# Kernel tuning notes

Measured on AMD Instinct MI355X. Metric: run time of the kernel, lower is better.

The kernel has to match this reference:

```python
import jax, jax.numpy as jnp
import numpy as np

H = 256; HEADS = 4; DH = H // HEADS; LAYERS = 2; FEAT = 7
N = 20000; L = 32; E = 640000


def _ln(x, g, b, eps=1e-5):
    mu = x.mean(-1, keepdims=True)
    var = ((x - mu) ** 2).mean(-1, keepdims=True)
    return (x - mu) / jnp.sqrt(var + eps) * g + b


def setup_inputs() -> dict:
    key = jax.random.key(0)
    ks = jax.random.split(key, 12)
    s = 0.05
    nrm = lambda k, shp: jax.random.normal(k, shp, jnp.float32) * s
    return {
        "literal_reprs": jax.random.normal(ks[0], (N, L, H), jnp.float32),
        "clause_features": jax.random.uniform(ks[1], (N, FEAT), jnp.float32),
        "mask": jax.random.randint(ks[2], (N, L), 0, 2) == 1,
        "adjacency": jax.random.randint(ks[3], (2, E), 0, N),
        "pe_w1": nrm(ks[4], (FEAT, H)), "pe_b1": jnp.zeros((H,), jnp.float32),
        "pe_w2": nrm(ks[5], (H, H)), "pe_b2": jnp.zeros((H,), jnp.float32),
        "attn_in_w": nrm(ks[6], (H, 3 * H)), "attn_in_b": jnp.zeros((3 * H,), jnp.float32),
        "attn_out_w": nrm(ks[7], (H, H)), "attn_out_b": jnp.zeros((H,), jnp.float32),
        "attn_ln_g": jnp.ones((H,), jnp.float32), "attn_ln_b": jnp.zeros((H,), jnp.float32),
        "gate_w": nrm(ks[8], (2 * H, H)), "gate_b": jnp.zeros((H,), jnp.float32),
        "trans_w": nrm(ks[9], (2 * H, H)), "trans_b": jnp.zeros((H,), jnp.float32),
        "fus_ln_g": jnp.ones((H,), jnp.float32), "fus_ln_b": jnp.zeros((H,), jnp.float32),
        "mp_w": nrm(ks[10], (LAYERS, 2 * H, H)), "mp_b": jnp.zeros((LAYERS, H), jnp.float32),
        "mp_ln_g": jnp.ones((LAYERS, H), jnp.float32), "mp_ln_b": jnp.zeros((LAYERS, H), jnp.float32),
    }


def reference(literal_reprs, clause_features, mask, adjacency,
              pe_w1, pe_b1, pe_w2, pe_b2,
              attn_in_w, attn_in_b, attn_out_w, attn_out_b,
              attn_ln_g, attn_ln_b, gate_w, gate_b, trans_w, trans_b,
              fus_ln_g, fus_ln_b, mp_w, mp_b, mp_ln_g, mp_ln_b):
    n, l, h = literal_reprs.shape
    # clause property encoder (shared by query and fusion path)
    enc = jnp.maximum(clause_features @ pe_w1 + pe_b1, 0.0) @ pe_w2 + pe_b2  # (N, H)
    # single-query multi-head attention over literals
    wq, wk, wv = attn_in_w[:, :H], attn_in_w[:, H:2 * H], attn_in_w[:, 2 * H:]
    bq, bk, bv = attn_in_b[:H], attn_in_b[H:2 * H], attn_in_b[2 * H:]
    q = ((enc @ wq + bq) * (1.0 / np.sqrt(DH))).reshape(n, HEADS, DH)
    k = (literal_reprs @ wk + bk).reshape(n, l, HEADS, DH)
    v = (literal_reprs @ wv + bv).reshape(n, l, HEADS, DH)
    scores = jnp.einsum('nhd,nlhd->nhl', q, k)
    kpm = ~mask  # True = masked out
    all_masked = jnp.all(kpm, axis=1)
    kpm = kpm.at[:, 0].set(jnp.where(all_masked, False, kpm[:, 0]))  # unmask pos 0 for fully-masked rows
    scores = jnp.where(kpm[:, None, :], -jnp.inf, scores)
    attn = jax.nn.softmax(scores, axis=-1)
    ctx = jnp.einsum('nhl,nlhd->nhd', attn, v).reshape(n, h) @ attn_out_w + attn_out_b
    ctx = jnp.where(all_masked[:, None], 0.0, ctx)  # zero fully-masked rows
    attn_repr = _ln(ctx + enc, attn_ln_g, attn_ln_b)
    # masked mean-pool residual
    mf = mask.astype(literal_reprs.dtype)[:, :, None]
    lit_mean = (literal_reprs * mf).sum(1) / jnp.maximum(mf.sum(1), 1.0)
    attn_repr = attn_repr + lit_mean
    # gated fusion
    combined = jnp.concatenate([attn_repr, enc], axis=-1)
    gate = jax.nn.sigmoid(combined @ gate_w + gate_b)
    transform = combined @ trans_w + trans_b
    x = _ln(gate * attn_repr + (1.0 - gate) * transform, fus_ln_g, fus_ln_b)
    # inter-clause message passing
    src, dst = adjacency[0], adjacency[1]
    ones = jnp.ones((src.shape[0],), x.dtype)
    for i in range(LAYERS):
        agg = jax.ops.segment_sum(x[src], dst, num_segments=n)
        cnt = jax.ops.segment_sum(ones, dst, num_segments=n)
        agg = agg / jnp.maximum(cnt, 1.0)[:, None]
        upd = jnp.maximum(jnp.concatenate([x, agg], axis=-1) @ mp_w[i] + mp_b[i], 0.0)
        x = _ln(x + upd, mp_ln_g[i], mp_ln_b[i])
    return x
```

## Files before the change

### kernel.cpp

```cpp
#include <hip/hip_runtime.h>
#include <math.h>

#define H 256
#define L 32
#define HEADS 4
#define FEAT 7
#define LN_EPS 1e-5f

typedef __attribute__((ext_vector_type(8))) short bf16x8;
typedef __attribute__((ext_vector_type(4))) float f32x4;
typedef __attribute__((ext_vector_type(4))) float fvec4;

__device__ __forceinline__ float wave_reduce_sum64(float v) {
#pragma unroll
  for (int m = 32; m >= 1; m >>= 1) v += __shfl_xor(v, m, 64);
  return v;
}

__device__ __forceinline__ short bf16rne(float f) {
  unsigned u = __float_as_uint(f);
  unsigned r = (u + 0x7FFFu + ((u >> 16) & 1u)) >> 16;
  return (short)r;
}

__device__ __forceinline__ float bf2f(short s) {
  return __uint_as_float(((unsigned)(unsigned short)s) << 16);
}

__global__ __launch_bounds__(256) void k_prep(
    const float* __restrict__ pe_w2, const float* __restrict__ aiw, const float* __restrict__ aow,
    const float* __restrict__ aib, const float* __restrict__ aob,
    const float* __restrict__ gate_w, const float* __restrict__ trans_w, const float* __restrict__ mp_w,
    short* __restrict__ w2P, short* __restrict__ wqpP, short* __restrict__ wbigP,
    short* __restrict__ gwP, short* __restrict__ twP, short* __restrict__ mp0P, short* __restrict__ mp1P,
    float* __restrict__ bias_p, float* __restrict__ bias_out, int* __restrict__ hist, int n) {
  const int bb = blockIdx.x;
  const int tid = threadIdx.x;
  if (bb < 32) {
    const int t = bb * 256 + tid;
    const int lane = t & 63;
    const int ks = (t >> 6) & 7;
    const int tcol = (t >> 6) >> 3;
    const int j = tcol * 16 + (lane & 15);
    const int k0 = ks * 32 + (lane >> 4) * 8;
    short v[8];
#pragma unroll
    for (int i = 0; i < 8; ++i) v[i] = bf16rne(pe_w2[(size_t)(k0 + i) * 256 + j]);
    *(int4*)&w2P[(size_t)t * 8] = *(int4*)v;
  } else if (bb < 160) {
    const int t = (bb - 32) * 256 + tid;
    const int lane = t & 63;
    const int ks = (t >> 6) & 7;
    const int tcol = t >> 9;
    const int col = tcol * 16 + (lane & 15);
    const int h = col >> 8, c = col & 255;
    const int k0 = ks * 32 + (lane >> 4) * 8;
    short v[8];
#pragma unroll
    for (int i = 0; i < 8; ++i) {
      const int k = k0 + i;
      float s = 0.f;
      for (int d = 0; d < 64; d += 4) {
        const float4 qa = *(const float4*)&aiw[(size_t)k * 768 + h * 64 + d];
        const float4 ka = *(const float4*)&aiw[(size_t)c * 768 + 256 + h * 64 + d];
        s = fmaf(qa.x, ka.x, fmaf(qa.y, ka.y, fmaf(qa.z, ka.z, fmaf(qa.w, ka.w, s))));
      }
      v[i] = bf16rne(0.125f * s);
    }
    *(int4*)&wqpP[(size_t)t * 8] = *(int4*)v;
  } else if (bb < 288) {
    const int t = (bb - 160) * 256 + tid;
    const int lane = t & 63;
    const int ks = (t >> 6) & 31;
    const int tcol = t >> 11;
    const int j = tcol * 16 + (lane & 15);
    const int k0 = ks * 32 + (lane >> 4) * 8;
    short v[8];
#pragma unroll
    for (int i = 0; i < 8; ++i) {
      const int k = k0 + i;
      const int c = k >> 2, h = k & 3;
      float s = 0.f;
      for (int d = 0; d < 64; ++d)
        s = fmaf(aiw[(size_t)c * 768 + 512 + h * 64 + d], aow[(size_t)(h * 64 + d) * 256 + j], s);
      v[i] = bf16rne(s);
    }
    *(int4*)&wbigP[(size_t)t * 8] = *(int4*)v;
  } else if (bb < 544) {
    const int sub = bb - 288;
    const int mi = sub >> 6;
    const float* W = (mi == 0) ? gate_w : (mi == 1) ? trans_w : (mi == 2) ? mp_w : (mp_w + 512 * 256);
    short* P = (mi == 0) ? gwP : (mi == 1) ? twP : (mi == 2) ? mp0P : mp1P;
    const int t = (sub & 63) * 256 + tid;
    const int lane = t & 63;
    const int ks = (t >> 6) & 15;
    const int tcol = (t >> 6) >> 4;
    const int j = tcol * 16 + (lane & 15);
    const int k0 = ks * 32 + (lane >> 4) * 8;
    short v[8];
#pragma unroll
    for (int i = 0; i < 8; ++i) v[i] = bf16rne(W[(size_t)(k0 + i) * 256 + j]);
    *(int4*)&P[(size_t)t * 8] = *(int4*)v;
  } else if (bb < 548) {
    const int col = (bb - 544) * 256 + tid;
    const int h = col >> 8, c = col & 255;
    float s = 0.f;
    for (int d = 0; d < 64; ++d)
      s = fmaf(aib[h * 64 + d], aiw[(size_t)c * 768 + 256 + h * 64 + d], s);
    bias_p[col] = 0.125f * s;
  } else if (bb == 548) {
    const int j = tid;
    float s = aob[j];
    for (int e2 = 0; e2 < 256; ++e2) s = fmaf(aib[512 + e2], aow[(size_t)e2 * 256 + j], s);
    bias_out[j] = s;
  } else {
    const int i = (bb - 549) * 256 + tid;
    if (i < n) hist[i] = 0;
  }
}

__global__ __launch_bounds__(256) void k_enc_mfma(
    const float* __restrict__ cf, const float* __restrict__ pe_w1, const float* __restrict__ pe_b1,
    const short* __restrict__ w2P, const float* __restrict__ pe_b2,
    const short* __restrict__ wqpP, const float* __restrict__ bias_p,
    short* __restrict__ enc_bf16, short* __restrict__ p_bf16, int n) {
  __shared__ float cfs[32][FEAT];
  __shared__ short h1[32][264];
  __shared__ short encS[32][264];
  const int tid = threadIdx.x;
  const int lane = tid & 63, w = tid >> 6;
  const int n0 = blockIdx.x * 32;
  for (int idx = tid; idx < 32 * FEAT; idx += 256) cfs[idx / FEAT][idx % FEAT] = cf[(size_t)n0 * FEAT + idx];
  __syncthreads();
  {
    const int j = tid;
    float wv[FEAT];
#pragma unroll
    for (int f = 0; f < FEAT; ++f) wv[f] = pe_w1[f * H + j];
    const float b1v = pe_b1[j];
    for (int r = 0; r < 32; ++r) {
      float s = b1v;
#pragma unroll
      for (int f = 0; f < FEAT; ++f) s = fmaf(cfs[r][f], wv[f], s);
      h1[r][j] = bf16rne(fmaxf(s, 0.f));
    }
  }
  __syncthreads();
  const int arow = lane & 15;
  const int koff = (lane >> 4) * 8;
  {
    f32x4 acc[2][4];
#pragma unroll
    for (int rt = 0; rt < 2; ++rt)
#pragma unroll
      for (int ct = 0; ct < 4; ++ct) acc[rt][ct] = (f32x4)0.f;
#pragma unroll
    for (int ks = 0; ks < 8; ++ks) {
      const int k0 = ks * 32 + koff;
      const bf16x8 a0 = *(const bf16x8*)&h1[arow][k0];
      const bf16x8 a1 = *(const bf16x8*)&h1[16 + arow][k0];
#pragma unroll
      for (int ct = 0; ct < 4; ++ct) {
        const size_t fo = (((size_t)(w * 4 + ct) * 8 + ks) * 64 + lane) * 8;
        const bf16x8 b = *(const bf16x8*)&w2P[fo];
        acc[0][ct] = __builtin_amdgcn_mfma_f32_16x16x32_bf16(a0, b, acc[0][ct], 0, 0, 0);
        acc[1][ct] = __builtin_amdgcn_mfma_f32_16x16x32_bf16(a1, b, acc[1][ct], 0, 0, 0);
      }
    }
#pragma unroll
    for (int rt = 0; rt < 2; ++rt)
#pragma unroll
      for (int ct = 0; ct < 4; ++ct) {
        const int col = w * 64 + ct * 16 + (lane & 15);
        const float b2v = pe_b2[col];
#pragma unroll
        for (int i = 0; i < 4; ++i) {
          const int row = rt * 16 + (lane >> 4) * 4 + i;
          const short bv = bf16rne(acc[rt][ct][i] + b2v);
          encS[row][col] = bv;
          enc_bf16[(size_t)(n0 + row) * H + col] = bv;
        }
      }
  }
  __syncthreads();
#pragma unroll
  for (int chunk = 0; chunk < 2; ++chunk) {
    f32x4 acc[2][8];
#pragma unroll
    for (int rt = 0; rt < 2; ++rt)
#pragma unroll
      for (int c8 = 0; c8 < 8; ++c8) acc[rt][c8] = (f32x4)0.f;
#pragma unroll
    for (int ks = 0; ks < 8; ++ks) {
      const int k0 = ks * 32 + koff;
      const bf16x8 a0 = *(const bf16x8*)&encS[arow][k0];
      const bf16x8 a1 = *(const bf16x8*)&encS[16 + arow][k0];
#pragma unroll
      for (int c8 = 0; c8 < 8; ++c8) {
        const int tcol = w * 16 + chunk * 8 + c8;
        const size_t fo = (((size_t)tcol * 8 + ks) * 64 + lane) * 8;
        const bf16x8 b = *(const bf16x8*)&wqpP[fo];
        acc[0][c8] = __builtin_amdgcn_mfma_f32_16x16x32_bf16(a0, b, acc[0][c8], 0, 0, 0);
        acc[1][c8] = __builtin_amdgcn_mfma_f32_16x16x32_bf16(a1, b, acc[1][c8], 0, 0, 0);
      }
    }
#pragma unroll
    for (int rt = 0; rt < 2; ++rt)
#pragma unroll
      for (int c8 = 0; c8 < 8; ++c8) {
        const int col = w * 256 + (chunk * 8 + c8) * 16 + (lane & 15);
        const float bp = bias_p[col];
#pragma unroll
        for (int i = 0; i < 4; ++i) {
          const int row = rt * 16 + (lane >> 4) * 4 + i;
          p_bf16[(size_t)(n0 + row) * 1024 + col] = bf16rne(acc[rt][c8][i] + bp);
        }
      }
  }
}

__global__ __launch_bounds__(256) void k_attn(
    const float* __restrict__ lit, const int* __restrict__ mask,
    const short* __restrict__ p_in, short* __restrict__ m_out,
    short* __restrict__ litmean_bf, int* __restrict__ flags, int n) {
  __shared__ short lit_bs[32][264];
  __shared__ float attn_s[32][4];
  __shared__ int validS[32];
  __shared__ int nvalidS;
  const int j = threadIdx.x;
  const int nn = blockIdx.x;
  const fvec4* litrow4 = (const fvec4*)(lit + (size_t)nn * (L * H));
#pragma unroll
  for (int t = 0; t < 8; ++t) {
    const int q = t * 256 + j;
    const int idx = q << 2;
    const int r = idx >> 8, c = idx & 255;
    const fvec4 f = __builtin_nontemporal_load(&litrow4[q]);
    short4 hv;
    hv.x = bf16rne(f.x); hv.y = bf16rne(f.y); hv.z = bf16rne(f.z); hv.w = bf16rne(f.w);
    *(short4*)&lit_bs[r][c] = hv;
  }
  if (j < 32) validS[j] = (mask[(size_t)nn * L + j] != 0) ? 1 : 0;
  __syncthreads();
  if (j == 0) {
    int c = 0;
#pragma unroll
    for (int l = 0; l < 32; ++l) c += validS[l];
    nvalidS = c;
  }
  __syncthreads();
  const int nvalid = nvalidS;
  const bool allm = (nvalid == 0);
  if (j < 64) {
    const int lane = j;
    f32x4 sc0 = (f32x4)0.f, sc1 = (f32x4)0.f;
    const int hh = lane & 3;
    const int krow = (lane >> 4) * 8;
    const short* prow = p_in + (size_t)nn * 1024 + hh * 256;
#pragma unroll
    for (int ks = 0; ks < 8; ++ks) {
      const bf16x8 a = *(const bf16x8*)&prow[ks * 32 + krow];
      const bf16x8 b0 = *(const bf16x8*)&lit_bs[lane & 15][ks * 32 + krow];
      const bf16x8 b1 = *(const bf16x8*)&lit_bs[16 + (lane & 15)][ks * 32 + krow];
      sc0 = __builtin_amdgcn_mfma_f32_16x16x32_bf16(a, b0, sc0, 0, 0, 0);
      sc1 = __builtin_amdgcn_mfma_f32_16x16x32_bf16(a, b1, sc1, 0, 0, 0);
    }
    if (lane < 16) {
      const int l0 = lane, l1 = 16 + lane;
      const bool ok0 = validS[l0] || (allm && l0 == 0);
      const bool ok1 = validS[l1] != 0;
#pragma unroll
      for (int i = 0; i < 4; ++i) {
        float s0 = ok0 ? sc0[i] : -INFINITY;
        float s1 = ok1 ? sc1[i] : -INFINITY;
        float mx = fmaxf(s0, s1);
#pragma unroll
        for (int m = 8; m >= 1; m >>= 1) mx = fmaxf(mx, __shfl_xor(mx, m, 16));
        float e0 = ok0 ? __expf(s0 - mx) : 0.f;
        float e1 = ok1 ? __expf(s1 - mx) : 0.f;
        float sm = e0 + e1;
#pragma unroll
        for (int m = 8; m >= 1; m >>= 1) sm += __shfl_xor(sm, m, 16);
        const float inv = 1.f / sm;
        attn_s[l0][i] = e0 * inv;
        attn_s[l1][i] = e1 * inv;
      }
    }
  }
  __syncthreads();
  {
    const float inv = 1.f / fmaxf((float)nvalid, 1.f);
    float lm = 0.f;
    float mm0 = 0.f, mm1 = 0.f, mm2 = 0.f, mm3 = 0.f;
#pragma unroll
    for (int l = 0; l < 32; ++l) {
      const float lv = bf2f(lit_bs[l][j]);
      if (validS[l]) lm += lv;
      const float4 av = *(const float4*)&attn_s[l][0];
      mm0 = fmaf(av.x, lv, mm0);
      mm1 = fmaf(av.y, lv, mm1);
      mm2 = fmaf(av.z, lv, mm2);
      mm3 = fmaf(av.w, lv, mm3);
    }
    litmean_bf[(size_t)nn * H + j] = bf16rne(lm * inv);
    short4 mv;
    mv.x = bf16rne(mm0); mv.y = bf16rne(mm1); mv.z = bf16rne(mm2); mv.w = bf16rne(mm3);
    *(short4*)&m_out[(size_t)nn * 1024 + j * 4] = mv;
  }
  if (j == 0) flags[nn] = allm ? 1 : 0;
}

__global__ __launch_bounds__(256) void k_fused(
    const short* __restrict__ m_bf16, const short* __restrict__ wbigP, const float* __restrict__ bias_out,
    const short* __restrict__ enc_bf16, const short* __restrict__ litmean_bf, const int* __restrict__ flags,
    const float* __restrict__ ag, const float* __restrict__ ab,
    const short* __restrict__ gwP, const short* __restrict__ twP,
    const float* __restrict__ gb, const float* __restrict__ tb,
    const float* __restrict__ fg, const float* __restrict__ fb,
    short* __restrict__ xout_bf, int n) {
  __shared__ short As[32][520];
  __shared__ float v_s[32][260];
  __shared__ float mu_s[32], sg_s[32];
  __shared__ int flagS[32];
  const int tid = threadIdx.x;
  const int lane = tid & 63, w = tid >> 6;
  const int n0 = blockIdx.x * 32;
  for (int q8 = tid; q8 < 32 * 32; q8 += 256) {
    const int idx = q8 << 3;
    const int r = idx >> 8, c = idx & 255;
    *(int4*)&As[r][256 + c] = *(const int4*)&enc_bf16[(size_t)(n0 + r) * H + c];
  }
  if (tid < 32) flagS[tid] = flags[n0 + tid];
  const int arow = lane & 15;
  const int koff = (lane >> 4) * 8;
  f32x4 acc[2][4];
#pragma unroll
  for (int rt = 0; rt < 2; ++rt)
#pragma unroll
    for (int ct = 0; ct < 4; ++ct) acc[rt][ct] = (f32x4)0.f;
#pragma unroll 8
  for (int ks = 0; ks < 32; ++ks) {
    const size_t abase = (size_t)(n0 + arow) * 1024 + ks * 32 + koff;
    const bf16x8 a0 = *(const bf16x8*)&m_bf16[abase];
    const bf16x8 a1 = *(const bf16x8*)&m_bf16[abase + 16 * 1024];
#pragma unroll
    for (int ct = 0; ct < 4; ++ct) {
      const size_t fo = (((size_t)(w * 4 + ct) * 32 + ks) * 64 + lane) * 8;
      const bf16x8 bw = *(const bf16x8*)&wbigP[fo];
      acc[0][ct] = __builtin_amdgcn_mfma_f32_16x16x32_bf16(a0, bw, acc[0][ct], 0, 0, 0);
      acc[1][ct] = __builtin_amdgcn_mfma_f32_16x16x32_bf16(a1, bw, acc[1][ct], 0, 0, 0);
    }
  }
  __syncthreads();
#pragma unroll
  for (int rt = 0; rt < 2; ++rt)
#pragma unroll
    for (int ct = 0; ct < 4; ++ct) {
      const int col = w * 64 + ct * 16 + (lane & 15);
      const float bo = bias_out[col];
#pragma unroll
      for (int i = 0; i < 4; ++i) {
        const int row = rt * 16 + (lane >> 4) * 4 + i;
        const float o = flagS[row] ? 0.f : (acc[rt][ct][i] + bo);
        v_s[row][col] = o + bf2f(As[row][256 + col]);
      }
    }
  __syncthreads();
  for (int r = w; r < 32; r += 4) {
    float ps = 0.f, pq = 0.f;
#pragma unroll
    for (int t = 0; t < 4; ++t) {
      float v = v_s[r][lane + 64 * t];
      ps += v;
      pq = fmaf(v, v, pq);
    }
    ps = wave_reduce_sum64(ps);
    pq = wave_reduce_sum64(pq);
    if (lane == 0) {
      float mu = ps * (1.f / H);
      mu_s[r] = mu;
      sg_s[r] = rsqrtf(pq * (1.f / H) - mu * mu + LN_EPS);
    }
  }
  __syncthreads();
  {
    const float agv = ag[tid], abv = ab[tid];
    for (int r = 0; r < 32; ++r) {
      const float val = (v_s[r][tid] - mu_s[r]) * sg_s[r] * agv + abv +
                        bf2f(litmean_bf[(size_t)(n0 + r) * H + tid]);
      As[r][tid] = bf16rne(val);
    }
  }
  __syncthreads();
  f32x4 accg[2][4], acct[2][4];
#pragma unroll
  for (int rt = 0; rt < 2; ++rt)
#pragma unroll
    for (int ct = 0; ct < 4; ++ct) { accg[rt][ct] = (f32x4)0.f; acct[rt][ct] = (f32x4)0.f; }
#pragma unroll 4
  for (int ks = 0; ks < 16; ++ks) {
    const int k0 = ks * 32 + koff;
    const bf16x8 a0 = *(const bf16x8*)&As[arow][k0];
    const bf16x8 a1 = *(const bf16x8*)&As[16 + arow][k0];
#pragma unroll
    for (int ct = 0; ct < 4; ++ct) {
      const size_t fo = (((size_t)(w * 4 + ct) * 16 + ks) * 64 + lane) * 8;
      const bf16x8 bg = *(const bf16x8*)&gwP[fo];
      const bf16x8 bt = *(const bf16x8*)&twP[fo];
      accg[0][ct] = __builtin_amdgcn_mfma_f32_16x16x32_bf16(a0, bg, accg[0][ct], 0, 0, 0);
      accg[1][ct] = __builtin_amdgcn_mfma_f32_16x16x32_bf16(a1, bg, accg[1][ct], 0, 0, 0);
      acct[0][ct] = __builtin_amdgcn_mfma_f32_16x16x32_bf16(a0, bt, acct[0][ct], 0, 0, 0);
      acct[1][ct] = __builtin_amdgcn_mfma_f32_16x16x32_bf16(a1, bt, acct[1][ct], 0, 0, 0);
    }
  }
#pragma unroll
  for (int rt = 0; rt < 2; ++rt)
#pragma unroll
    for (int ct = 0; ct < 4; ++ct) {
      const int col = w * 64 + ct * 16 + (lane & 15);
      const float gbv = gb[col], tbv = tb[col];
#pragma unroll
      for (int i = 0; i < 4; ++i) {
        const int rl = rt * 16 + (lane >> 4) * 4 + i;
        const float gate = 1.f / (1.f + __expf(-(accg[rt][ct][i] + gbv)));
        const float tr = acct[rt][ct][i] + tbv;
        const float a = bf2f(As[rl][col]);
        v_s[rl][col] = fmaf(gate, a - tr, tr);
      }
    }
  __syncthreads();
  for (int r = w; r < 32; r += 4) {
    float ps = 0.f, pq = 0.f;
#pragma unroll
    for (int t = 0; t < 4; ++t) {
      float v = v_s[r][lane + 64 * t];
      ps += v;
      pq = fmaf(v, v, pq);
    }
    ps = wave_reduce_sum64(ps);
    pq = wave_reduce_sum64(pq);
    if (lane == 0) {
      float mu = ps * (1.f / H);
      mu_s[r] = mu;
      sg_s[r] = rsqrtf(pq * (1.f / H) - mu * mu + LN_EPS);
    }
  }
  __syncthreads();
  {
    const float fgv = fg[tid], fbv = fb[tid];
    for (int r = 0; r < 32; ++r)
      xout_bf[(size_t)(n0 + r) * H + tid] = bf16rne((v_s[r][tid] - mu_s[r]) * sg_s[r] * fgv + fbv);
  }
}

__global__ __launch_bounds__(256) void k_mp_mfma(
    const short* __restrict__ xin_bf, const short* __restrict__ agg_bf,
    const short* __restrict__ wP, const float* __restrict__ bias,
    const float* __restrict__ g, const float* __restrict__ b,
    float* __restrict__ xout_f32, short* __restrict__ xout_bf, int n) {
  __shared__ float v_s[32][260];
  __shared__ float mu_s[32], sg_s[32];
  const int tid = threadIdx.x;
  const int lane = tid & 63, w = tid >> 6;
  const int n0 = blockIdx.x * 32;
  const int arow = lane & 15;
  const int koff = (lane >> 4) * 8;
  f32x4 acc[2][4];
#pragma unroll
  for (int rt = 0; rt < 2; ++rt)
#pragma unroll
    for (int ct = 0; ct < 4; ++ct) acc[rt][ct] = (f32x4)0.f;
  const short* xr0 = xin_bf + (size_t)(n0 + arow) * H;
  const short* xr1 = xin_bf + (size_t)(n0 + 16 + arow) * H;
  const short* gr0 = agg_bf + (size_t)(n0 + arow) * H;
  const short* gr1 = agg_bf + (size_t)(n0 + 16 + arow) * H;
#pragma unroll
  for (int ks = 0; ks < 8; ++ks) {
    const bf16x8 a0 = *(const bf16x8*)&xr0[ks * 32 + koff];
    const bf16x8 a1 = *(const bf16x8*)&xr1[ks * 32 + koff];
#pragma unroll
    for (int ct = 0; ct < 4; ++ct) {
      const size_t fo = (((size_t)(w * 4 + ct) * 16 + ks) * 64 + lane) * 8;
      const bf16x8 bw = *(const bf16x8*)&wP[fo];
      acc[0][ct] = __builtin_amdgcn_mfma_f32_16x16x32_bf16(a0, bw, acc[0][ct], 0, 0, 0);
      acc[1][ct] = __builtin_amdgcn_mfma_f32_16x16x32_bf16(a1, bw, acc[1][ct], 0, 0, 0);
    }
  }
#pragma unroll
  for (int ks = 8; ks < 16; ++ks) {
    const bf16x8 a0 = *(const bf16x8*)&gr0[(ks - 8) * 32 + koff];
    const bf16x8 a1 = *(const bf16x8*)&gr1[(ks - 8) * 32 + koff];
#pragma unroll
    for (int ct = 0; ct < 4; ++ct) {
      const size_t fo = (((size_t)(w * 4 + ct) * 16 + ks) * 64 + lane) * 8;
      const bf16x8 bw = *(const bf16x8*)&wP[fo];
      acc[0][ct] = __builtin_amdgcn_mfma_f32_16x16x32_bf16(a0, bw, acc[0][ct], 0, 0, 0);
      acc[1][ct] = __builtin_amdgcn_mfma_f32_16x16x32_bf16(a1, bw, acc[1][ct], 0, 0, 0);
    }
  }
#pragma unroll
  for (int rt = 0; rt < 2; ++rt)
#pragma unroll
    for (int ct = 0; ct < 4; ++ct) {
      const int col = w * 64 + ct * 16 + (lane & 15);
      const float bsv = bias[col];
#pragma unroll
      for (int i = 0; i < 4; ++i) {
        const int rl = rt * 16 + (lane >> 4) * 4 + i;
        const float u = fmaxf(acc[rt][ct][i] + bsv, 0.f);
        v_s[rl][col] = bf2f(xin_bf[(size_t)(n0 + rl) * H + col]) + u;
      }
    }
  __syncthreads();
  for (int r = w; r < 32; r += 4) {
    float ps = 0.f, pq = 0.f;
#pragma unroll
    for (int t = 0; t < 4; ++t) {
      float v = v_s[r][lane + 64 * t];
      ps += v;
      pq = fmaf(v, v, pq);
    }
    ps = wave_reduce_sum64(ps);
    pq = wave_reduce_sum64(pq);
    if (lane == 0) {
      float mu = ps * (1.f / H);
      mu_s[r] = mu;
      sg_s[r] = rsqrtf(pq * (1.f / H) - mu * mu + LN_EPS);
    }
  }
  __syncthreads();
  const float gv = g[tid], bv = b[tid];
  for (int r = 0; r < 32; ++r) {
    const float val = (v_s[r][tid] - mu_s[r]) * sg_s[r] * gv + bv;
    if (xout_f32) xout_f32[(size_t)(n0 + r) * H + tid] = val;
    if (xout_bf) xout_bf[(size_t)(n0 + r) * H + tid] = bf16rne(val);
  }
}

__global__ void k_hist(const int* __restrict__ dst, int* __restrict__ hist, int e) {
  int i = blockIdx.x * blockDim.x + threadIdx.x;
  if (i < e) atomicAdd(&hist[dst[i]], 1);
}

__global__ __launch_bounds__(1024) void k_scan(
    const int* __restrict__ hist, int* __restrict__ row_ptr, int* __restrict__ cursor, int n, int e) {
  __shared__ int part[1024];
  const int t = threadIdx.x;
  const int chunk = (n + 1023) / 1024;
  const int lo = t * chunk;
  const int hi = min(lo + chunk, n);
  int s = 0;
  for (int i = lo; i < hi; ++i) s += hist[i];
  part[t] = s;
  __syncthreads();
  for (int d = 1; d < 1024; d <<= 1) {
    int v = (t >= d) ? part[t - d] : 0;
    __syncthreads();
    part[t] += v;
    __syncthreads();
  }
  int run = (t > 0) ? part[t - 1] : 0;
  for (int i = lo; i < hi; ++i) {
    row_ptr[i] = run;
    cursor[i] = run;
    run += hist[i];
  }
  if (t == 1023) row_ptr[n] = e;
}

__global__ void k_fill(const int* __restrict__ adj, int* __restrict__ cursor,
                       int* __restrict__ edge_src, int e) {
  int i = blockIdx.x * blockDim.x + threadIdx.x;
  if (i < e) {
    int s = adj[i], d = adj[e + i];
    int pos = atomicAdd(&cursor[d], 1);
    edge_src[pos] = s;
  }
}

__global__ __launch_bounds__(256) void k_gather(
    const short* __restrict__ x, const int* __restrict__ edge_src, const int* __restrict__ row_ptr,
    short* __restrict__ agg, int n) {
  const int wid = threadIdx.x >> 6;
  const int lane = threadIdx.x & 63;
  const int d = blockIdx.x * 4 + wid;
  if (d >= n) return;
  const int beg = row_ptr[d], end = row_ptr[d + 1];
  float4 acc = {0.f, 0.f, 0.f, 0.f};
  int i = beg;
  for (; i + 8 <= end; i += 8) {
    short4 v[8];
#pragma unroll
    for (int u = 0; u < 8; ++u) {
      const int s = edge_src[i + u];
      v[u] = *(const short4*)(x + (size_t)s * H + lane * 4);
    }
#pragma unroll
    for (int u = 0; u < 8; ++u) {
      acc.x += bf2f(v[u].x);
      acc.y += bf2f(v[u].y);
      acc.z += bf2f(v[u].z);
      acc.w += bf2f(v[u].w);
    }
  }
  for (; i < end; ++i) {
    const int s = edge_src[i];
    const short4 v = *(const short4*)(x + (size_t)s * H + lane * 4);
    acc.x += bf2f(v.x); acc.y += bf2f(v.y); acc.z += bf2f(v.z); acc.w += bf2f(v.w);
  }
  const float inv = 1.f / fmaxf((float)(end - beg), 1.f);
  short4 o;
  o.x = bf16rne(acc.x * inv); o.y = bf16rne(acc.y * inv);
  o.z = bf16rne(acc.z * inv); o.w = bf16rne(acc.w * inv);
  *(short4*)(agg + (size_t)d * H + lane * 4) = o;
}

extern "C" void kernel_launch(void* const* d_in, const int* in_sizes, int n_in,
                              void* d_out, int out_size, void* d_ws, size_t ws_size,
                              hipStream_t stream) {
  const float* lit = (const float*)d_in[0];
  const float* cf = (const float*)d_in[1];
  const int* mask = (const int*)d_in[2];
  const int* adj = (const int*)d_in[3];
  const float* pe_w1 = (const float*)d_in[4];
  const float* pe_b1 = (const float*)d_in[5];
  const float* pe_w2 = (const float*)d_in[6];
  const float* pe_b2 = (const float*)d_in[7];
  const float* aiw = (const float*)d_in[8];
  const float* aib = (const float*)d_in[9];
  const float* aow = (const float*)d_in[10];
  const float* aob = (const float*)d_in[11];
  const float* attn_ln_g = (const float*)d_in[12];
  const float* attn_ln_b = (const float*)d_in[13];
  const float* gate_w = (const float*)d_in[14];
  const float* gate_b = (const float*)d_in[15];
  const float* trans_w = (const float*)d_in[16];
  const float* trans_b = (const float*)d_in[17];
  const float* fus_ln_g = (const float*)d_in[18];
  const float* fus_ln_b = (const float*)d_in[19];
  const float* mp_w = (const float*)d_in[20];
  const float* mp_b = (const float*)d_in[21];
  const float* mp_ln_g = (const float*)d_in[22];
  const float* mp_ln_b = (const float*)d_in[23];

  const int n = in_sizes[1] / FEAT;
  const int e = in_sizes[3] / 2;

  float* ws = (float*)d_ws;
  size_t off = 0;
  short* enc_bf16 = (short*)(ws + off); off += (size_t)n * 128;
  short* pm_bf16 = (short*)(ws + off); off += (size_t)n * 512;
  short* litmean_bf = (short*)(ws + off); off += (size_t)n * 128;
  short* x0_bf = (short*)(ws + off); off += (size_t)n * 128;
  short* x1_bf = (short*)(ws + off); off += (size_t)n * 128;
  short* agg_bf = (short*)(ws + off); off += (size_t)n * 128;
  int* flags = (int*)(ws + off); off += n;
  int* hist = (int*)(ws + off); off += n;
  int* row_ptr = (int*)(ws + off); off += n + 2;
  int* cursor = (int*)(ws + off); off += n;
  int* edge_src = (int*)(ws + off); off += e;
  short* w2P = (short*)(ws + off); off += 256 * 256 / 2;
  short* wqpP = (short*)(ws + off); off += 256 * 1024 / 2;
  short* wbigP = (short*)(ws + off); off += 1024 * 256 / 2;
  short* gwP = (short*)(ws + off); off += 512 * 256 / 2;
  short* twP = (short*)(ws + off); off += 512 * 256 / 2;
  short* mp0P = (short*)(ws + off); off += 512 * 256 / 2;
  short* mp1P = (short*)(ws + off); off += 512 * 256 / 2;
  float* bias_p = ws + off; off += 1024;
  float* bias_out = ws + off; off += 256;

  dim3 blk(256);
  const int histBlocks = (n + 255) / 256;
  k_prep<<<549 + histBlocks, blk, 0, stream>>>(pe_w2, aiw, aow, aib, aob, gate_w, trans_w, mp_w,
                                               w2P, wqpP, wbigP, gwP, twP, mp0P, mp1P,
                                               bias_p, bias_out, hist, n);

  k_enc_mfma<<<n / 32, blk, 0, stream>>>(cf, pe_w1, pe_b1, w2P, pe_b2, wqpP, bias_p, enc_bf16, pm_bf16, n);
  k_attn<<<n, blk, 0, stream>>>(lit, mask, pm_bf16, pm_bf16, litmean_bf, flags, n);

  k_hist<<<(e + 255) / 256, blk, 0, stream>>>(adj + e, hist, e);
  k_scan<<<1, 1024, 0, stream>>>(hist, row_ptr, cursor, n, e);
  k_fill<<<(e + 255) / 256, blk, 0, stream>>>(adj, cursor, edge_src, e);

  k_fused<<<n / 32, blk, 0, stream>>>(pm_bf16, wbigP, bias_out, enc_bf16, litmean_bf, flags,
                                      attn_ln_g, attn_ln_b, gwP, twP, gate_b, trans_b,
                                      fus_ln_g, fus_ln_b, x0_bf, n);
  k_gather<<<(n + 3) / 4, blk, 0, stream>>>(x0_bf, edge_src, row_ptr, agg_bf, n);
  k_mp_mfma<<<n / 32, blk, 0, stream>>>(x0_bf, agg_bf, mp0P, mp_b, mp_ln_g, mp_ln_b,
                                        nullptr, x1_bf, n);
  k_gather<<<(n + 3) / 4, blk, 0, stream>>>(x1_bf, edge_src, row_ptr, agg_bf, n);
  k_mp_mfma<<<n / 32, blk, 0, stream>>>(x1_bf, agg_bf, mp1P, mp_b + 256, mp_ln_g + 256,
                                        mp_ln_b + 256, (float*)d_out, nullptr, n);
}
```

Baseline: 577.4 us.

## Fold CSR build kernels into encoder, attention and fusion launches as extra blocks

The histogram, scan and fill kernels that build the CSR adjacency are removed. Their work now runs as extra blocks appended to the encoder, attention and fused kernels, which saves three launches and lets the CSR work overlap with the compute kernels. The scan now runs as a single 256-thread block inside the attention grid, so each thread walks a longer serial chunk. Launch ordering on the stream still keeps hist before scan before fill.

Measured after the change: 540.1 us. 6.5% less time.

```diff
diff --git a/kernel.cpp b/kernel.cpp
--- a/kernel.cpp
+++ b/kernel.cpp
@@ -123,11 +123,18 @@
     const float* __restrict__ cf, const float* __restrict__ pe_w1, const float* __restrict__ pe_b1,
     const short* __restrict__ w2P, const float* __restrict__ pe_b2,
     const short* __restrict__ wqpP, const float* __restrict__ bias_p,
-    short* __restrict__ enc_bf16, short* __restrict__ p_bf16, int n) {
+    short* __restrict__ enc_bf16, short* __restrict__ p_bf16, int n,
+    const int* __restrict__ adj_dst, int* __restrict__ hist, int e) {
+  const int tid = threadIdx.x;
+  const int nEnc = n / 32;
+  if ((int)blockIdx.x >= nEnc) {
+    const int i = ((int)blockIdx.x - nEnc) * 256 + tid;
+    if (i < e) atomicAdd(&hist[adj_dst[i]], 1);
+    return;
+  }
   __shared__ float cfs[32][FEAT];
   __shared__ short h1[32][264];
   __shared__ short encS[32][264];
-  const int tid = threadIdx.x;
   const int lane = tid & 63, w = tid >> 6;
   const int n0 = blockIdx.x * 32;
   for (int idx = tid; idx < 32 * FEAT; idx += 256) cfs[idx / FEAT][idx % FEAT] = cf[(size_t)n0 * FEAT + idx];
@@ -222,13 +229,38 @@
 __global__ __launch_bounds__(256) void k_attn(
     const float* __restrict__ lit, const int* __restrict__ mask,
     const short* __restrict__ p_in, short* __restrict__ m_out,
-    short* __restrict__ litmean_bf, int* __restrict__ flags, int n) {
+    short* __restrict__ litmean_bf, int* __restrict__ flags, int n,
+    const int* __restrict__ hist, int* __restrict__ row_ptr, int* __restrict__ cursor, int e) {
+  const int j = threadIdx.x;
+  const int nn = blockIdx.x;
+  if (nn == n) {
+    __shared__ int part[256];
+    const int chunk = (n + 255) / 256;
+    const int lo = j * chunk;
+    const int hi = min(lo + chunk, n);
+    int s = 0;
+    for (int i = lo; i < hi; ++i) s += hist[i];
+    part[j] = s;
+    __syncthreads();
+    for (int d = 1; d < 256; d <<= 1) {
+      int v = (j >= d) ? part[j - d] : 0;
+      __syncthreads();
+      part[j] += v;
+      __syncthreads();
+    }
+    int run = (j > 0) ? part[j - 1] : 0;
+    for (int i = lo; i < hi; ++i) {
+      row_ptr[i] = run;
+      cursor[i] = run;
+      run += hist[i];
+    }
+    if (j == 255) row_ptr[n] = e;
+    return;
+  }
   __shared__ short lit_bs[32][264];
   __shared__ float attn_s[32][4];
   __shared__ int validS[32];
   __shared__ int nvalidS;
-  const int j = threadIdx.x;
-  const int nn = blockIdx.x;
   const fvec4* litrow4 = (const fvec4*)(lit + (size_t)nn * (L * H));
 #pragma unroll
   for (int t = 0; t < 8; ++t) {
@@ -317,12 +349,23 @@
     const short* __restrict__ gwP, const short* __restrict__ twP,
     const float* __restrict__ gb, const float* __restrict__ tb,
     const float* __restrict__ fg, const float* __restrict__ fb,
-    short* __restrict__ xout_bf, int n) {
+    short* __restrict__ xout_bf, int n,
+    const int* __restrict__ adj, int* __restrict__ cursor, int* __restrict__ edge_src, int e) {
+  const int tid = threadIdx.x;
+  const int nFused = n / 32;
+  if ((int)blockIdx.x >= nFused) {
+    const int i = ((int)blockIdx.x - nFused) * 256 + tid;
+    if (i < e) {
+      const int s = adj[i], d = adj[e + i];
+      const int pos = atomicAdd(&cursor[d], 1);
+      edge_src[pos] = s;
+    }
+    return;
+  }
   __shared__ short As[32][520];
   __shared__ float v_s[32][260];
   __shared__ float mu_s[32], sg_s[32];
   __shared__ int flagS[32];
-  const int tid = threadIdx.x;
   const int lane = tid & 63, w = tid >> 6;
   const int n0 = blockIdx.x * 32;
   for (int q8 = tid; q8 < 32 * 32; q8 += 256) {
@@ -534,47 +577,6 @@
     const float val = (v_s[r][tid] - mu_s[r]) * sg_s[r] * gv + bv;
     if (xout_f32) xout_f32[(size_t)(n0 + r) * H + tid] = val;
     if (xout_bf) xout_bf[(size_t)(n0 + r) * H + tid] = bf16rne(val);
-  }
-}
-
-__global__ void k_hist(const int* __restrict__ dst, int* __restrict__ hist, int e) {
-  int i = blockIdx.x * blockDim.x + threadIdx.x;
-  if (i < e) atomicAdd(&hist[dst[i]], 1);
-}
-
-__global__ __launch_bounds__(1024) void k_scan(
-    const int* __restrict__ hist, int* __restrict__ row_ptr, int* __restrict__ cursor, int n, int e) {
-  __shared__ int part[1024];
-  const int t = threadIdx.x;
-  const int chunk = (n + 1023) / 1024;
-  const int lo = t * chunk;
-  const int hi = min(lo + chunk, n);
-  int s = 0;
-  for (int i = lo; i < hi; ++i) s += hist[i];
-  part[t] = s;
-  __syncthreads();
-  for (int d = 1; d < 1024; d <<= 1) {
-    int v = (t >= d) ? part[t - d] : 0;
-    __syncthreads();
-    part[t] += v;
-    __syncthreads();
-  }
-  int run = (t > 0) ? part[t - 1] : 0;
-  for (int i = lo; i < hi; ++i) {
-    row_ptr[i] = run;
-    cursor[i] = run;
-    run += hist[i];
-  }
-  if (t == 1023) row_ptr[n] = e;
-}
-
-__global__ void k_fill(const int* __restrict__ adj, int* __restrict__ cursor,
-                       int* __restrict__ edge_src, int e) {
-  int i = blockIdx.x * blockDim.x + threadIdx.x;
-  if (i < e) {
-    int s = adj[i], d = adj[e + i];
-    int pos = atomicAdd(&cursor[d], 1);
-    edge_src[pos] = s;
   }
 }
 
@@ -671,20 +673,19 @@
 
   dim3 blk(256);
   const int histBlocks = (n + 255) / 256;
+  const int csrBlocks = (e + 255) / 256;
   k_prep<<<549 + histBlocks, blk, 0, stream>>>(pe_w2, aiw, aow, aib, aob, gate_w, trans_w, mp_w,
                                                w2P, wqpP, wbigP, gwP, twP, mp0P, mp1P,
                                                bias_p, bias_out, hist, n);
 
-  k_enc_mfma<<<n / 32, blk, 0, stream>>>(cf, pe_w1, pe_b1, w2P, pe_b2, wqpP, bias_p, enc_bf16, pm_bf16, n);
-  k_attn<<<n, blk, 0, stream>>>(lit, mask, pm_bf16, pm_bf16, litmean_bf, flags, n);
-
-  k_hist<<<(e + 255) / 256, blk, 0, stream>>>(adj + e, hist, e);
-  k_scan<<<1, 1024, 0, stream>>>(hist, row_ptr, cursor, n, e);
-  k_fill<<<(e + 255) / 256, blk, 0, stream>>>(adj, cursor, edge_src, e);
-
-  k_fused<<<n / 32, blk, 0, stream>>>(pm_bf16, wbigP, bias_out, enc_bf16, litmean_bf, flags,
-                                      attn_ln_g, attn_ln_b, gwP, twP, gate_b, trans_b,
-                                      fus_ln_g, fus_ln_b, x0_bf, n);
+  k_enc_mfma<<<n / 32 + csrBlocks, blk, 0, stream>>>(cf, pe_w1, pe_b1, w2P, pe_b2, wqpP, bias_p,
+                                                     enc_bf16, pm_bf16, n, adj + e, hist, e);
+  k_attn<<<n + 1, blk, 0, stream>>>(lit, mask, pm_bf16, pm_bf16, litmean_bf, flags, n,
+                                    hist, row_ptr, cursor, e);
+  k_fused<<<n / 32 + csrBlocks, blk, 0, stream>>>(pm_bf16, wbigP, bias_out, enc_bf16, litmean_bf, flags,
+                                                  attn_ln_g, attn_ln_b, gwP, twP, gate_b, trans_b,
+                                                  fus_ln_g, fus_ln_b, x0_bf, n,
+                                                  adj, cursor, edge_src, e);
   k_gather<<<(n + 3) / 4, blk, 0, stream>>>(x0_bf, edge_src, row_ptr, agg_bf, n);
   k_mp_mfma<<<n / 32, blk, 0, stream>>>(x0_bf, agg_bf, mp0P, mp_b, mp_ln_g, mp_ln_b,
                                         nullptr, x1_bf, n);
```
